# Kernel optimization log

Hardware: AMD Instinct MI355X
Metric: run time of the kernel (lower is better)

The kernel has to match this reference:

```python
import jax, jax.numpy as jnp
import numpy as np

B, S, H, D = 1, 2048, 16, 128
HID = H * D  # 2048
EPS = 1e-6


def setup_inputs() -> dict:
    key = jax.random.key(0)
    ks = jax.random.split(key, 6)
    sc = 1.0 / np.sqrt(HID)
    t = jnp.arange(S, dtype=jnp.float32)[:, None]
    inv = 1.0 / (10000.0 ** (jnp.arange(D // 2, dtype=jnp.float32) / (D // 2)))
    ang = t * inv[None, :]
    return {
        "hidden_states": jax.random.normal(ks[0], (B, S, HID), jnp.float32),
        "freqs_cos": jnp.cos(ang),
        "freqs_sin": jnp.sin(ang),
        "w_qkv": jax.random.normal(ks[1], (HID, 3 * HID), jnp.float32) * sc,
        "b_qkv": jnp.zeros((3 * HID,), jnp.float32),
        "w_norm_q": jnp.ones((HID,), jnp.float32),
        "w_norm_k": jnp.ones((HID,), jnp.float32),
        "w_out": jax.random.normal(ks[2], (HID, HID), jnp.float32) * sc,
        "b_out": jnp.zeros((HID,), jnp.float32),
    }


def _rmsnorm(x, w):
    var = jnp.mean(jnp.square(x), axis=-1, keepdims=True)
    return x * jax.lax.rsqrt(var + EPS) * w


def _rope(x, cos, sin):
    # x: [B, H, S, D]; cos/sin: [S, D//2], interleaved pair rotation
    xr = x.reshape(*x.shape[:-1], D // 2, 2)
    x1, x2 = xr[..., 0], xr[..., 1]
    c = cos[None, None, :, :]
    s = sin[None, None, :, :]
    o1 = x1 * c - x2 * s
    o2 = x1 * s + x2 * c
    return jnp.stack([o1, o2], axis=-1).reshape(x.shape)


def reference(hidden_states, freqs_cos, freqs_sin, w_qkv, b_qkv,
              w_norm_q, w_norm_k, w_out, b_out):
    qkv = hidden_states @ w_qkv + b_qkv  # [B, S, 3*HID]
    q, k, v = jnp.split(qkv, 3, axis=-1)
    q = _rmsnorm(q, w_norm_q).reshape(B, S, H, D).transpose(0, 2, 1, 3)
    k = _rmsnorm(k, w_norm_k).reshape(B, S, H, D).transpose(0, 2, 1, 3)
    v = v.reshape(B, S, H, D).transpose(0, 2, 1, 3)
    q = _rope(q, freqs_cos, freqs_sin)
    k = _rope(k, freqs_cos, freqs_sin)
    scale = 1.0 / np.sqrt(D)
    scores = jnp.einsum("bhqd,bhkd->bhqk", q, k) * scale
    attn = jax.nn.softmax(scores, axis=-1)
    out = jnp.einsum("bhqk,bhkd->bhqd", attn, v)
    out = out.transpose(0, 2, 1, 3).reshape(B, S, HID)
    return out @ w_out + b_out
```

## Files before the change

kernel.cpp:

```cpp
#include <hip/hip_runtime.h>
#include <math.h>

typedef unsigned short u16;
typedef __bf16 bf16x8 __attribute__((ext_vector_type(8)));
typedef float f32x4 __attribute__((ext_vector_type(4)));
typedef unsigned short u16x8 __attribute__((ext_vector_type(8)));

#define SLEN 2048
#define HIDN 2048
#define NH   16
#define DHD  128

static __device__ __forceinline__ float bf2f(u16 u) {
  unsigned int i = ((unsigned int)u) << 16;
  return __builtin_bit_cast(float, i);
}
static __device__ __forceinline__ u16 f2bf(float f) {
  unsigned int x = __builtin_bit_cast(unsigned int, f);
  unsigned int r = x + 0x7fffu + ((x >> 16) & 1u);
  return (u16)(r >> 16);
}
static __device__ __forceinline__ void gload_lds16(const u16* g, u16* l) {
  __builtin_amdgcn_global_load_lds((const __attribute__((address_space(1))) void*)g,
                                   (__attribute__((address_space(3))) void*)l,
                                   16, 0, 0);
}

__global__ __launch_bounds__(256) void prep(const float* __restrict__ wqkv,
                                            const float* __restrict__ wout,
                                            const float* __restrict__ hs,
                                            u16* __restrict__ wqkvT,
                                            u16* __restrict__ woutT,
                                            u16* __restrict__ hsB) {
  const int lin = blockIdx.x;
  const int t = threadIdx.x;
  if (lin >= 4096) {
    int i = ((lin - 4096) * 256 + t) * 8;
    f32x4 a = *(const f32x4*)&hs[i];
    f32x4 b = *(const f32x4*)&hs[i + 4];
    u16x8 v;
#pragma unroll
    for (int j = 0; j < 4; ++j) { v[j] = f2bf(a[j]); v[4 + j] = f2bf(b[j]); }
    *(u16x8*)&hsB[i] = v;
    return;
  }
  const float* in;
  u16* out;
  int istride, ostride, bx, by;
  if (lin < 3072) {
    in = wqkv; out = wqkvT; istride = 6144; ostride = 2048;
    bx = lin & 31; by = lin >> 5;
  } else {
    in = wout; out = woutT; istride = 2048; ostride = 2048;
    int idx = lin - 3072;
    bx = idx & 31; by = idx >> 5;
  }
  __shared__ float tl[64][65];
  const int r0 = bx * 64, c0 = by * 64;
#pragma unroll
  for (int it = 0; it < 4; ++it) {
    int row = it * 16 + (t >> 4);
    int col = (t & 15) * 4;
    f32x4 v = *(const f32x4*)&in[(size_t)(r0 + row) * istride + c0 + col];
    tl[row][col] = v[0]; tl[row][col + 1] = v[1];
    tl[row][col + 2] = v[2]; tl[row][col + 3] = v[3];
  }
  __syncthreads();
#pragma unroll
  for (int it = 0; it < 2; ++it) {
    int orow = it * 32 + (t >> 3);
    int ocol = (t & 7) * 8;
    u16x8 v;
#pragma unroll
    for (int j = 0; j < 8; ++j) v[j] = f2bf(tl[ocol + j][orow]);
    *(u16x8*)&out[(size_t)(c0 + orow) * ostride + r0 + ocol] = v;
  }
}

static __device__ __forceinline__ void xcd_map(int lin, int N, int* pbx, int* pby) {
  const int nby = N >> 7;
  const int cby = nby >> 3;
  const int xcd = lin & 7, idx = lin >> 3;
  *pby = xcd * cby + (idx % cby);
  *pbx = idx / cby;
}

__global__ __launch_bounds__(256) void gemm_sb(const u16* __restrict__ A,
                                               const u16* __restrict__ BT,
                                               const float* __restrict__ bias,
                                               float* Cf, u16* Cb,
                                               int M, int N, int K) {
  int bx, by;
  xcd_map(blockIdx.x, N, &bx, &by);

  __shared__ u16 lA[128 * 64];
  __shared__ u16 lB[128 * 64];
  const int t = threadIdx.x;
  const int lane = t & 63, w = t >> 6;
  const int g = lane >> 4, l16 = lane & 15;
  const int wr = w >> 1, wc = w & 1;
  const u16* Ab = A + (size_t)bx * 128 * K;
  const u16* Bb = BT + (size_t)by * 128 * K;

  f32x4 acc[4][4];
#pragma unroll
  for (int mi = 0; mi < 4; ++mi)
#pragma unroll
    for (int ni = 0; ni < 4; ++ni) acc[mi][ni] = (f32x4)(0.0f);

  for (int k0 = 0; k0 < K; k0 += 64) {
    __syncthreads();
#pragma unroll
    for (int i = 0; i < 4; ++i) {
      int e = t * 8 + i * 2048;
      int row = e >> 6;
      int col16 = (e & 63) >> 3;
      int scol = (col16 ^ (row & 7)) * 8;
      gload_lds16(Ab + (size_t)row * K + k0 + scol, &lA[e]);
      gload_lds16(Bb + (size_t)row * K + k0 + scol, &lB[e]);
    }
    __syncthreads();
#pragma unroll
    for (int kk = 0; kk < 2; ++kk) {
      bf16x8 af[4], bfr[4];
#pragma unroll
      for (int mi = 0; mi < 4; ++mi) {
        int row = wr * 64 + mi * 16 + l16;
        af[mi] = *(const bf16x8*)&lA[row * 64 + (((4 * kk + g) ^ (l16 & 7)) << 3)];
      }
#pragma unroll
      for (int ni = 0; ni < 4; ++ni) {
        int row = wc * 64 + ni * 16 + l16;
        bfr[ni] = *(const bf16x8*)&lB[row * 64 + (((4 * kk + g) ^ (l16 & 7)) << 3)];
      }
#pragma unroll
      for (int mi = 0; mi < 4; ++mi)
#pragma unroll
        for (int ni = 0; ni < 4; ++ni)
          acc[mi][ni] = __builtin_amdgcn_mfma_f32_16x16x32_bf16(af[mi], bfr[ni],
                                                                acc[mi][ni], 0, 0, 0);
    }
  }

#pragma unroll
  for (int ni = 0; ni < 4; ++ni) {
    int n = by * 128 + wc * 64 + ni * 16 + l16;
    float bv = bias[n];
#pragma unroll
    for (int mi = 0; mi < 4; ++mi) {
      int m = bx * 128 + wr * 64 + mi * 16 + 4 * g;
#pragma unroll
      for (int r = 0; r < 4; ++r) {
        float v = acc[mi][ni][r] + bv;
        if (Cf) Cf[(size_t)(m + r) * N + n] = v;
        else    Cb[(size_t)(m + r) * N + n] = f2bf(v);
      }
    }
  }
}

__global__ __launch_bounds__(256) void gemm_db(const u16* __restrict__ A,
                                               const u16* __restrict__ BT,
                                               const float* __restrict__ bias,
                                               float* Cf, u16* Cb,
                                               int M, int N, int K) {
  int bx, by;
  xcd_map(blockIdx.x, N, &bx, &by);

  __shared__ u16 lA[2][128 * 64];
  __shared__ u16 lB[2][128 * 64];
  const int t = threadIdx.x;
  const int lane = t & 63, w = t >> 6;
  const int g = lane >> 4, l16 = lane & 15;
  const int wr = w >> 1, wc = w & 1;
  const u16* Ab = A + (size_t)bx * 128 * K;
  const u16* Bb = BT + (size_t)by * 128 * K;

  f32x4 acc[4][4];
#pragma unroll
  for (int mi = 0; mi < 4; ++mi)
#pragma unroll
    for (int ni = 0; ni < 4; ++ni) acc[mi][ni] = (f32x4)(0.0f);

#pragma unroll
  for (int i = 0; i < 4; ++i) {
    int e = t * 8 + i * 2048;
    int row = e >> 6;
    int col16 = (e & 63) >> 3;
    int scol = (col16 ^ (row & 7)) * 8;
    gload_lds16(Ab + (size_t)row * K + scol, &lA[0][e]);
    gload_lds16(Bb + (size_t)row * K + scol, &lB[0][e]);
  }
  __syncthreads();

  const int nk = K >> 6;
  int cur = 0;
  for (int kt = 0; kt < nk; ++kt) {
    if (kt + 1 < nk) {
      const int k1 = (kt + 1) << 6;
#pragma unroll
      for (int i = 0; i < 4; ++i) {
        int e = t * 8 + i * 2048;
        int row = e >> 6;
        int col16 = (e & 63) >> 3;
        int scol = (col16 ^ (row & 7)) * 8;
        gload_lds16(Ab + (size_t)row * K + k1 + scol, &lA[cur ^ 1][e]);
        gload_lds16(Bb + (size_t)row * K + k1 + scol, &lB[cur ^ 1][e]);
      }
    }
#pragma unroll
    for (int kk = 0; kk < 2; ++kk) {
      bf16x8 af[4], bfr[4];
#pragma unroll
      for (int mi = 0; mi < 4; ++mi) {
        int row = wr * 64 + mi * 16 + l16;
        af[mi] = *(const bf16x8*)&lA[cur][row * 64 + (((4 * kk + g) ^ (l16 & 7)) << 3)];
      }
#pragma unroll
      for (int ni = 0; ni < 4; ++ni) {
        int row = wc * 64 + ni * 16 + l16;
        bfr[ni] = *(const bf16x8*)&lB[cur][row * 64 + (((4 * kk + g) ^ (l16 & 7)) << 3)];
      }
#pragma unroll
      for (int mi = 0; mi < 4; ++mi)
#pragma unroll
        for (int ni = 0; ni < 4; ++ni)
          acc[mi][ni] = __builtin_amdgcn_mfma_f32_16x16x32_bf16(af[mi], bfr[ni],
                                                                acc[mi][ni], 0, 0, 0);
    }
    __syncthreads();
    cur ^= 1;
  }

#pragma unroll
  for (int ni = 0; ni < 4; ++ni) {
    int n = by * 128 + wc * 64 + ni * 16 + l16;
    float bv = bias[n];
#pragma unroll
    for (int mi = 0; mi < 4; ++mi) {
      int m = bx * 128 + wr * 64 + mi * 16 + 4 * g;
#pragma unroll
      for (int r = 0; r < 4; ++r) {
        float v = acc[mi][ni][r] + bv;
        if (Cf) Cf[(size_t)(m + r) * N + n] = v;
        else    Cb[(size_t)(m + r) * N + n] = f2bf(v);
      }
    }
  }
}

__global__ __launch_bounds__(256) void mid(const u16* __restrict__ qkv,
                                           const float* __restrict__ fcos,
                                           const float* __restrict__ fsin,
                                           const float* __restrict__ wq,
                                           const float* __restrict__ wk,
                                           u16* __restrict__ Qr,
                                           u16* __restrict__ Kr,
                                           u16* __restrict__ Vt) {
  const int lin = blockIdx.x;
  const int t = threadIdx.x;

  if (lin >= 2048) {
    __shared__ u16 tl[64][72];
    int idx = lin - 2048;
    int bx = idx & 31;
    int byy = (idx >> 5) & 1;
    int z = idx >> 6;
    const u16* in = qkv + 4096 + (size_t)z * 128;
    u16* out = Vt + (size_t)z * 262144;
    const int r0 = bx * 64, c0 = byy * 64;
#pragma unroll
    for (int it = 0; it < 2; ++it) {
      int row = it * 32 + (t >> 3);
      int col = (t & 7) * 8;
      *(u16x8*)&tl[row][col] =
          *(const u16x8*)&in[(size_t)(r0 + row) * 6144 + c0 + col];
    }
    __syncthreads();
#pragma unroll
    for (int it = 0; it < 2; ++it) {
      int orow = it * 32 + (t >> 3);
      int ocol = (t & 7) * 8;
      u16x8 v;
#pragma unroll
      for (int j = 0; j < 8; ++j) v[j] = tl[ocol + j][orow];
      *(u16x8*)&out[(size_t)(c0 + orow) * 2048 + r0 + ocol] = v;
    }
    return;
  }

  const int s = lin;
  const int lane = t & 63, w = t >> 6;
  __shared__ float red[2][4];
  const u16* row = qkv + (size_t)s * (3 * HIDN);

  u16x8 xq = *(const u16x8*)&row[t * 8];
  u16x8 xk = *(const u16x8*)&row[HIDN + t * 8];
  float fq[8], fk[8];
  float ssq = 0.f, ssk = 0.f;
#pragma unroll
  for (int j = 0; j < 8; ++j) {
    fq[j] = bf2f(xq[j]); ssq += fq[j] * fq[j];
    fk[j] = bf2f(xk[j]); ssk += fk[j] * fk[j];
  }
#pragma unroll
  for (int off = 32; off >= 1; off >>= 1) {
    ssq += __shfl_xor(ssq, off);
    ssk += __shfl_xor(ssk, off);
  }
  if (lane == 0) { red[0][w] = ssq; red[1][w] = ssk; }
  __syncthreads();
  float sq = red[0][0] + red[0][1] + red[0][2] + red[0][3];
  float sk = red[1][0] + red[1][1] + red[1][2] + red[1][3];
  float rq = rsqrtf(sq / (float)HIDN + 1e-6f);
  float rk = rsqrtf(sk / (float)HIDN + 1e-6f);

  f32x4 wq0 = *(const f32x4*)&wq[t * 8];
  f32x4 wq1 = *(const f32x4*)&wq[t * 8 + 4];
  f32x4 wk0 = *(const f32x4*)&wk[t * 8];
  f32x4 wk1 = *(const f32x4*)&wk[t * 8 + 4];
  float wqa[8] = {wq0[0], wq0[1], wq0[2], wq0[3], wq1[0], wq1[1], wq1[2], wq1[3]};
  float wka[8] = {wk0[0], wk0[1], wk0[2], wk0[3], wk1[0], wk1[1], wk1[2], wk1[3]};
  const int c0 = t * 8;
  const int h = c0 >> 7;
  const int d0 = c0 & 127;
  const int i0 = d0 >> 1;
  const float* cp = fcos + (size_t)s * (DHD / 2) + i0;
  const float* sp = fsin + (size_t)s * (DHD / 2) + i0;
  const float qscale = 0.12751744925f;

  u16x8 oq, ok;
#pragma unroll
  for (int p = 0; p < 4; ++p) {
    float c = cp[p], sn = sp[p];
    float q1 = fq[2 * p] * rq * wqa[2 * p];
    float q2 = fq[2 * p + 1] * rq * wqa[2 * p + 1];
    float k1 = fk[2 * p] * rk * wka[2 * p];
    float k2 = fk[2 * p + 1] * rk * wka[2 * p + 1];
    oq[2 * p]     = f2bf((q1 * c - q2 * sn) * qscale);
    oq[2 * p + 1] = f2bf((q1 * sn + q2 * c) * qscale);
    ok[2 * p]     = f2bf(k1 * c - k2 * sn);
    ok[2 * p + 1] = f2bf(k1 * sn + k2 * c);
  }
  size_t o = (size_t)h * SLEN * DHD + (size_t)s * DHD + d0;
  *(u16x8*)&Qr[o] = oq;
  *(u16x8*)&Kr[o] = ok;
}

__global__ __launch_bounds__(256) void attn_fwd(const u16* __restrict__ Qr,
                                                const u16* __restrict__ Kr,
                                                const u16* __restrict__ Vt,
                                                u16* __restrict__ out) {
  const int lin = blockIdx.x;
  const int xcd = lin & 7, idx = lin >> 3;
  const int h = xcd + ((idx >> 5) << 3);
  const int qb = idx & 31;
  const int t = threadIdx.x;
  const int lane = t & 63, w = t >> 6;
  const int g = lane >> 4, l16 = lane & 15;
  const int q0 = qb * 64 + w * 16;
  const u16* Qh = Qr + (size_t)h * SLEN * DHD;
  const u16* Kh = Kr + (size_t)h * SLEN * DHD;
  const u16* Vh = Vt + (size_t)h * DHD * SLEN;

  __shared__ u16 Kl[2][64 * 128];
  __shared__ u16 Vl[2][128 * 64];
  __shared__ u16 Pl[4][16][72];

  bf16x8 aq[4];
#pragma unroll
  for (int dk = 0; dk < 4; ++dk)
    aq[dk] = *(const bf16x8*)&Qh[(size_t)(q0 + l16) * DHD + dk * 32 + g * 8];

  f32x4 o[8];
#pragma unroll
  for (int df = 0; df < 8; ++df) o[df] = (f32x4)(0.0f);
  float m = -INFINITY, lsum = 0.f;

#pragma unroll
  for (int i = 0; i < 4; ++i) {
    int e = t * 8 + i * 2048;
    int kr = e >> 7, kc = (e & 127) >> 3;
    gload_lds16(Kh + (size_t)kr * DHD + ((kc ^ (kr & 7)) << 3), &Kl[0][e]);
    int vr = e >> 6, vc = (e & 63) >> 3;
    gload_lds16(Vh + (size_t)vr * SLEN + ((vc ^ (vr & 7)) << 3), &Vl[0][e]);
  }
  __syncthreads();

  int cur = 0;
  for (int kt = 0; kt < SLEN / 64; ++kt) {
    if (kt + 1 < SLEN / 64) {
      const int kv1 = (kt + 1) * 64;
#pragma unroll
      for (int i = 0; i < 4; ++i) {
        int e = t * 8 + i * 2048;
        int kr = e >> 7, kc = (e & 127) >> 3;
        gload_lds16(Kh + (size_t)(kv1 + kr) * DHD + ((kc ^ (kr & 7)) << 3),
                    &Kl[cur ^ 1][e]);
        int vr = e >> 6, vc = (e & 63) >> 3;
        gload_lds16(Vh + (size_t)vr * SLEN + kv1 + ((vc ^ (vr & 7)) << 3),
                    &Vl[cur ^ 1][e]);
      }
    }

    f32x4 s4[4];
#pragma unroll
    for (int nf = 0; nf < 4; ++nf) s4[nf] = (f32x4)(0.0f);
    __builtin_amdgcn_s_setprio(1);
#pragma unroll
    for (int nf = 0; nf < 4; ++nf) {
#pragma unroll
      for (int dk = 0; dk < 4; ++dk) {
        bf16x8 bk = *(const bf16x8*)&Kl[cur][(nf * 16 + l16) * 128 +
                                            (((dk * 4 + g) ^ (l16 & 7)) << 3)];
        s4[nf] = __builtin_amdgcn_mfma_f32_16x16x32_bf16(bk, aq[dk], s4[nf], 0, 0, 0);
      }
    }
    __builtin_amdgcn_s_setprio(0);
    float tm = s4[0][0];
#pragma unroll
    for (int nf = 0; nf < 4; ++nf)
#pragma unroll
      for (int r = 0; r < 4; ++r) tm = fmaxf(tm, s4[nf][r]);
    tm = fmaxf(tm, __shfl_xor(tm, 16));
    tm = fmaxf(tm, __shfl_xor(tm, 32));
    const bool nogrow = (tm <= m);
    const float mn = nogrow ? m : tm;
    float ls = 0.f;
#pragma unroll
    for (int nf = 0; nf < 4; ++nf)
#pragma unroll
      for (int r = 0; r < 4; ++r) {
        float p = exp2f(s4[nf][r] - mn);
        s4[nf][r] = p;
        ls += p;
      }
    ls += __shfl_xor(ls, 16);
    ls += __shfl_xor(ls, 32);
    if (__all(nogrow)) {
      lsum += ls;
    } else {
      float corr = exp2f(m - mn);
      m = mn;
      lsum = lsum * corr + ls;
#pragma unroll
      for (int r = 0; r < 4; ++r) {
        float cr = __shfl(corr, 20 * g + r);
#pragma unroll
        for (int df = 0; df < 8; ++df) o[df][r] *= cr;
      }
    }
#pragma unroll
    for (int nf = 0; nf < 4; ++nf)
#pragma unroll
      for (int r = 0; r < 4; ++r)
        Pl[w][l16][nf * 16 + 4 * g + r] = f2bf(s4[nf][r]);
#pragma unroll
    for (int ks = 0; ks < 2; ++ks) {
      bf16x8 ap = *(const bf16x8*)&Pl[w][l16][ks * 32 + g * 8];
      __builtin_amdgcn_s_setprio(1);
#pragma unroll
      for (int df = 0; df < 8; ++df) {
        bf16x8 bv = *(const bf16x8*)&Vl[cur][(df * 16 + l16) * 64 +
                                             (((ks * 4 + g) ^ (l16 & 7)) << 3)];
        o[df] = __builtin_amdgcn_mfma_f32_16x16x32_bf16(ap, bv, o[df], 0, 0, 0);
      }
      __builtin_amdgcn_s_setprio(0);
    }
    __syncthreads();
    cur ^= 1;
  }

  const float invq = 1.0f / lsum;
#pragma unroll
  for (int r = 0; r < 4; ++r) {
    float ir = __shfl(invq, 20 * g + r);
#pragma unroll
    for (int df = 0; df < 8; ++df)
      out[(size_t)(q0 + 4 * g + r) * HIDN + h * DHD + df * 16 + l16] =
          f2bf(o[df][r] * ir);
  }
}

extern "C" void kernel_launch(void* const* d_in, const int* in_sizes, int n_in,
                              void* d_out, int out_size, void* d_ws, size_t ws_size,
                              hipStream_t stream) {
  (void)in_sizes; (void)n_in; (void)out_size; (void)ws_size;
  const float* hs   = (const float*)d_in[0];
  const float* fc   = (const float*)d_in[1];
  const float* fs   = (const float*)d_in[2];
  const float* wqkv = (const float*)d_in[3];
  const float* bqkv = (const float*)d_in[4];
  const float* wnq  = (const float*)d_in[5];
  const float* wnk  = (const float*)d_in[6];
  const float* wout = (const float*)d_in[7];
  const float* bout = (const float*)d_in[8];
  float* out = (float*)d_out;
  char* ws = (char*)d_ws;

  u16* wqkvT = (u16*)(ws);
  u16* woutT = (u16*)(ws + 25165824);
  u16* qkv   = (u16*)(ws + 33554432);
  u16* hsB   = (u16*)(ws + 58720256);
  u16* Qr    = (u16*)(ws + 58720256);
  u16* Kr    = (u16*)(ws + 67108864);
  u16* Vt    = (u16*)(ws + 75497472);
  u16* attnO = (u16*)(ws + 83886080);

  prep<<<dim3(6144), 256, 0, stream>>>(wqkv, wout, hs, wqkvT, woutT, hsB);
  gemm_sb<<<dim3(768), 256, 0, stream>>>(hsB, wqkvT, bqkv, nullptr, qkv,
                                         2048, 6144, 2048);
  mid<<<dim3(3072), 256, 0, stream>>>(qkv, fc, fs, wnq, wnk, Qr, Kr, Vt);
  attn_fwd<<<dim3(512), 256, 0, stream>>>(Qr, Kr, Vt, attnO);
  gemm_db<<<dim3(256), 256, 0, stream>>>(attnO, woutT, bout, out, nullptr,
                                         2048, 2048, 2048);
}
```

Baseline: 201.4 us.

## Split attention over two KV halves and merge partials in a combine kernel

The attention kernel now splits each query block's key/value range into two halves, launching twice as many blocks, and writes unnormalized partial outputs plus per-row max and sum. A new combine kernel merges the two partials with a log-sum-exp style rescale. The double-buffered LDS prefetch is replaced by single-buffered loads with two barriers per tile, which cuts LDS use (more resident blocks) but removes load/compute overlap. It also adds an extra launch and extra global traffic for the partials, and stores the partials in bf16 before the merge.

```diff
diff --git a/kernel.cpp b/kernel.cpp
--- a/kernel.cpp
+++ b/kernel.cpp
@@ -347,24 +347,27 @@
   *(u16x8*)&Kr[o] = ok;
 }
 
-__global__ __launch_bounds__(256) void attn_fwd(const u16* __restrict__ Qr,
-                                                const u16* __restrict__ Kr,
-                                                const u16* __restrict__ Vt,
-                                                u16* __restrict__ out) {
+__global__ __launch_bounds__(256) void attn_split(const u16* __restrict__ Qr,
+                                                  const u16* __restrict__ Kr,
+                                                  const u16* __restrict__ Vt,
+                                                  u16* __restrict__ Op,
+                                                  float* __restrict__ ml) {
   const int lin = blockIdx.x;
   const int xcd = lin & 7, idx = lin >> 3;
-  const int h = xcd + ((idx >> 5) << 3);
-  const int qb = idx & 31;
+  const int split = idx & 1;
+  const int qb = (idx >> 1) & 31;
+  const int h = xcd + ((idx >> 6) << 3);
   const int t = threadIdx.x;
   const int lane = t & 63, w = t >> 6;
   const int g = lane >> 4, l16 = lane & 15;
   const int q0 = qb * 64 + w * 16;
+  const int kvbase = split << 10;
   const u16* Qh = Qr + (size_t)h * SLEN * DHD;
   const u16* Kh = Kr + (size_t)h * SLEN * DHD;
   const u16* Vh = Vt + (size_t)h * DHD * SLEN;
 
-  __shared__ u16 Kl[2][64 * 128];
-  __shared__ u16 Vl[2][128 * 64];
+  __shared__ u16 Kl[64 * 128];
+  __shared__ u16 Vl[128 * 64];
   __shared__ u16 Pl[4][16][72];
 
   bf16x8 aq[4];
@@ -377,31 +380,18 @@
   for (int df = 0; df < 8; ++df) o[df] = (f32x4)(0.0f);
   float m = -INFINITY, lsum = 0.f;
 
-#pragma unroll
-  for (int i = 0; i < 4; ++i) {
-    int e = t * 8 + i * 2048;
-    int kr = e >> 7, kc = (e & 127) >> 3;
-    gload_lds16(Kh + (size_t)kr * DHD + ((kc ^ (kr & 7)) << 3), &Kl[0][e]);
-    int vr = e >> 6, vc = (e & 63) >> 3;
-    gload_lds16(Vh + (size_t)vr * SLEN + ((vc ^ (vr & 7)) << 3), &Vl[0][e]);
-  }
-  __syncthreads();
-
-  int cur = 0;
-  for (int kt = 0; kt < SLEN / 64; ++kt) {
-    if (kt + 1 < SLEN / 64) {
-      const int kv1 = (kt + 1) * 64;
-#pragma unroll
-      for (int i = 0; i < 4; ++i) {
-        int e = t * 8 + i * 2048;
-        int kr = e >> 7, kc = (e & 127) >> 3;
-        gload_lds16(Kh + (size_t)(kv1 + kr) * DHD + ((kc ^ (kr & 7)) << 3),
-                    &Kl[cur ^ 1][e]);
-        int vr = e >> 6, vc = (e & 63) >> 3;
-        gload_lds16(Vh + (size_t)vr * SLEN + kv1 + ((vc ^ (vr & 7)) << 3),
-                    &Vl[cur ^ 1][e]);
-      }
-    }
+  for (int kt = 0; kt < 16; ++kt) {
+    const int kv0 = kvbase + kt * 64;
+    __syncthreads();
+#pragma unroll
+    for (int i = 0; i < 4; ++i) {
+      int e = t * 8 + i * 2048;
+      int kr = e >> 7, kc = (e & 127) >> 3;
+      gload_lds16(Kh + (size_t)(kv0 + kr) * DHD + ((kc ^ (kr & 7)) << 3), &Kl[e]);
+      int vr = e >> 6, vc = (e & 63) >> 3;
+      gload_lds16(Vh + (size_t)vr * SLEN + kv0 + ((vc ^ (vr & 7)) << 3), &Vl[e]);
+    }
+    __syncthreads();
 
     f32x4 s4[4];
 #pragma unroll
@@ -411,8 +401,8 @@
     for (int nf = 0; nf < 4; ++nf) {
 #pragma unroll
       for (int dk = 0; dk < 4; ++dk) {
-        bf16x8 bk = *(const bf16x8*)&Kl[cur][(nf * 16 + l16) * 128 +
-                                            (((dk * 4 + g) ^ (l16 & 7)) << 3)];
+        bf16x8 bk = *(const bf16x8*)&Kl[(nf * 16 + l16) * 128 +
+                                        (((dk * 4 + g) ^ (l16 & 7)) << 3)];
         s4[nf] = __builtin_amdgcn_mfma_f32_16x16x32_bf16(bk, aq[dk], s4[nf], 0, 0, 0);
       }
     }
@@ -461,25 +451,46 @@
       __builtin_amdgcn_s_setprio(1);
 #pragma unroll
       for (int df = 0; df < 8; ++df) {
-        bf16x8 bv = *(const bf16x8*)&Vl[cur][(df * 16 + l16) * 64 +
-                                             (((ks * 4 + g) ^ (l16 & 7)) << 3)];
+        bf16x8 bv = *(const bf16x8*)&Vl[(df * 16 + l16) * 64 +
+                                        (((ks * 4 + g) ^ (l16 & 7)) << 3)];
         o[df] = __builtin_amdgcn_mfma_f32_16x16x32_bf16(ap, bv, o[df], 0, 0, 0);
       }
       __builtin_amdgcn_s_setprio(0);
     }
-    __syncthreads();
-    cur ^= 1;
-  }
-
-  const float invq = 1.0f / lsum;
-#pragma unroll
-  for (int r = 0; r < 4; ++r) {
-    float ir = __shfl(invq, 20 * g + r);
+  }
+
+  const size_t ob = ((size_t)split * NH + h) * SLEN * DHD;
+#pragma unroll
+  for (int r = 0; r < 4; ++r)
 #pragma unroll
     for (int df = 0; df < 8; ++df)
-      out[(size_t)(q0 + 4 * g + r) * HIDN + h * DHD + df * 16 + l16] =
-          f2bf(o[df][r] * ir);
-  }
+      Op[ob + (size_t)(q0 + 4 * g + r) * DHD + df * 16 + l16] = f2bf(o[df][r]);
+  if (g == 0) {
+    size_t mb = (((size_t)split * NH + h) * SLEN + (q0 + l16)) * 2;
+    ml[mb] = m;
+    ml[mb + 1] = lsum;
+  }
+}
+
+__global__ __launch_bounds__(256) void combine(const u16* __restrict__ Op,
+                                               const float* __restrict__ ml,
+                                               u16* __restrict__ attnO) {
+  const int q = blockIdx.x, t = threadIdx.x;
+  const int h = t >> 4, d0 = (t & 15) * 8;
+  size_t mb0 = (((size_t)0 * NH + h) * SLEN + q) * 2;
+  size_t mb1 = (((size_t)1 * NH + h) * SLEN + q) * 2;
+  float m0 = ml[mb0], l0 = ml[mb0 + 1];
+  float m1 = ml[mb1], l1 = ml[mb1 + 1];
+  float ms = fmaxf(m0, m1);
+  float w0 = exp2f(m0 - ms), w1 = exp2f(m1 - ms);
+  float inv = 1.0f / (l0 * w0 + l1 * w1);
+  u16x8 a = *(const u16x8*)&Op[((size_t)0 * NH + h) * SLEN * DHD + (size_t)q * DHD + d0];
+  u16x8 b = *(const u16x8*)&Op[((size_t)1 * NH + h) * SLEN * DHD + (size_t)q * DHD + d0];
+  u16x8 v;
+#pragma unroll
+  for (int j = 0; j < 8; ++j)
+    v[j] = f2bf((bf2f(a[j]) * w0 + bf2f(b[j]) * w1) * inv);
+  *(u16x8*)&attnO[(size_t)q * HIDN + h * DHD + d0] = v;
 }
 
 extern "C" void kernel_launch(void* const* d_in, const int* in_sizes, int n_in,
@@ -506,12 +517,15 @@
   u16* Kr    = (u16*)(ws + 67108864);
   u16* Vt    = (u16*)(ws + 75497472);
   u16* attnO = (u16*)(ws + 83886080);
+  float* mlF = (float*)(ws);
+  u16* Op    = (u16*)(ws + 33554432);
 
   prep<<<dim3(6144), 256, 0, stream>>>(wqkv, wout, hs, wqkvT, woutT, hsB);
   gemm_sb<<<dim3(768), 256, 0, stream>>>(hsB, wqkvT, bqkv, nullptr, qkv,
                                          2048, 6144, 2048);
   mid<<<dim3(3072), 256, 0, stream>>>(qkv, fc, fs, wnq, wnk, Qr, Kr, Vt);
-  attn_fwd<<<dim3(512), 256, 0, stream>>>(Qr, Kr, Vt, attnO);
+  attn_split<<<dim3(1024), 256, 0, stream>>>(Qr, Kr, Vt, Op, mlF);
+  combine<<<dim3(2048), 256, 0, stream>>>(Op, mlF, attnO);
   gemm_db<<<dim3(256), 256, 0, stream>>>(attnO, woutT, bout, out, nullptr,
                                          2048, 2048, 2048);
 }
```

Measured after the change: 215.0 us. 6.8% more time.

## Double-buffer QKV GEMM LDS tiles with BK=32 prefetch pipeline

Applied to the files above, without the earlier changes.

Replaces the single-buffered BK=64 QKV projection GEMM with a double-buffered BK=32 version. The global-to-LDS loads for the next k-tile are issued before the MFMAs on the current tile, and the loop needs one barrier per iteration instead of two. The aim is to hide global load latency behind compute. In exchange there are twice as many k iterations, each doing half the MFMA work per barrier, and the swizzle becomes a 4-way XOR that may cause more LDS bank conflicts.

```diff
diff --git a/kernel.cpp b/kernel.cpp
--- a/kernel.cpp
+++ b/kernel.cpp
@@ -85,16 +85,16 @@
   *pbx = idx / cby;
 }
 
-__global__ __launch_bounds__(256) void gemm_sb(const u16* __restrict__ A,
-                                               const u16* __restrict__ BT,
-                                               const float* __restrict__ bias,
-                                               float* Cf, u16* Cb,
-                                               int M, int N, int K) {
+__global__ __launch_bounds__(256) void gemm_p32(const u16* __restrict__ A,
+                                                const u16* __restrict__ BT,
+                                                const float* __restrict__ bias,
+                                                float* Cf, u16* Cb,
+                                                int M, int N, int K) {
   int bx, by;
   xcd_map(blockIdx.x, N, &bx, &by);
 
-  __shared__ u16 lA[128 * 64];
-  __shared__ u16 lB[128 * 64];
+  __shared__ u16 lA[2][128 * 32];
+  __shared__ u16 lB[2][128 * 32];
   const int t = threadIdx.x;
   const int lane = t & 63, w = t >> 6;
   const int g = lane >> 4, l16 = lane & 15;
@@ -108,38 +108,51 @@
 #pragma unroll
     for (int ni = 0; ni < 4; ++ni) acc[mi][ni] = (f32x4)(0.0f);
 
-  for (int k0 = 0; k0 < K; k0 += 64) {
+#pragma unroll
+  for (int i = 0; i < 2; ++i) {
+    int e = t * 8 + i * 2048;
+    int row = e >> 5;
+    int c4 = (e & 31) >> 3;
+    int scol = (c4 ^ (row & 3)) * 8;
+    gload_lds16(Ab + (size_t)row * K + scol, &lA[0][e]);
+    gload_lds16(Bb + (size_t)row * K + scol, &lB[0][e]);
+  }
+  __syncthreads();
+
+  const int nk = K >> 5;
+  int cur = 0;
+  for (int kt = 0; kt < nk; ++kt) {
+    if (kt + 1 < nk) {
+      const int k1 = (kt + 1) << 5;
+#pragma unroll
+      for (int i = 0; i < 2; ++i) {
+        int e = t * 8 + i * 2048;
+        int row = e >> 5;
+        int c4 = (e & 31) >> 3;
+        int scol = (c4 ^ (row & 3)) * 8;
+        gload_lds16(Ab + (size_t)row * K + k1 + scol, &lA[cur ^ 1][e]);
+        gload_lds16(Bb + (size_t)row * K + k1 + scol, &lB[cur ^ 1][e]);
+      }
+    }
+    bf16x8 af[4], bfr[4];
+#pragma unroll
+    for (int mi = 0; mi < 4; ++mi) {
+      int row = wr * 64 + mi * 16 + l16;
+      af[mi] = *(const bf16x8*)&lA[cur][row * 32 + ((g ^ (row & 3)) << 3)];
+    }
+#pragma unroll
+    for (int ni = 0; ni < 4; ++ni) {
+      int row = wc * 64 + ni * 16 + l16;
+      bfr[ni] = *(const bf16x8*)&lB[cur][row * 32 + ((g ^ (row & 3)) << 3)];
+    }
+#pragma unroll
+    for (int mi = 0; mi < 4; ++mi)
+#pragma unroll
+      for (int ni = 0; ni < 4; ++ni)
+        acc[mi][ni] = __builtin_amdgcn_mfma_f32_16x16x32_bf16(af[mi], bfr[ni],
+                                                              acc[mi][ni], 0, 0, 0);
     __syncthreads();
-#pragma unroll
-    for (int i = 0; i < 4; ++i) {
-      int e = t * 8 + i * 2048;
-      int row = e >> 6;
-      int col16 = (e & 63) >> 3;
-      int scol = (col16 ^ (row & 7)) * 8;
-      gload_lds16(Ab + (size_t)row * K + k0 + scol, &lA[e]);
-      gload_lds16(Bb + (size_t)row * K + k0 + scol, &lB[e]);
-    }
-    __syncthreads();
-#pragma unroll
-    for (int kk = 0; kk < 2; ++kk) {
-      bf16x8 af[4], bfr[4];
-#pragma unroll
-      for (int mi = 0; mi < 4; ++mi) {
-        int row = wr * 64 + mi * 16 + l16;
-        af[mi] = *(const bf16x8*)&lA[row * 64 + (((4 * kk + g) ^ (l16 & 7)) << 3)];
-      }
-#pragma unroll
-      for (int ni = 0; ni < 4; ++ni) {
-        int row = wc * 64 + ni * 16 + l16;
-        bfr[ni] = *(const bf16x8*)&lB[row * 64 + (((4 * kk + g) ^ (l16 & 7)) << 3)];
-      }
-#pragma unroll
-      for (int mi = 0; mi < 4; ++mi)
-#pragma unroll
-        for (int ni = 0; ni < 4; ++ni)
-          acc[mi][ni] = __builtin_amdgcn_mfma_f32_16x16x32_bf16(af[mi], bfr[ni],
-                                                                acc[mi][ni], 0, 0, 0);
-    }
+    cur ^= 1;
   }
 
 #pragma unroll
@@ -508,8 +521,8 @@
   u16* attnO = (u16*)(ws + 83886080);
 
   prep<<<dim3(6144), 256, 0, stream>>>(wqkv, wout, hs, wqkvT, woutT, hsB);
-  gemm_sb<<<dim3(768), 256, 0, stream>>>(hsB, wqkvT, bqkv, nullptr, qkv,
-                                         2048, 6144, 2048);
+  gemm_p32<<<dim3(768), 256, 0, stream>>>(hsB, wqkvT, bqkv, nullptr, qkv,
+                                          2048, 6144, 2048);
   mid<<<dim3(3072), 256, 0, stream>>>(qkv, fc, fs, wnq, wnk, Qr, Kr, Vt);
   attn_fwd<<<dim3(512), 256, 0, stream>>>(Qr, Kr, Vt, attnO);
   gemm_db<<<dim3(256), 256, 0, stream>>>(attnO, woutT, bout, out, nullptr,
```

After: 202.7 us. Within noise of the previous version (+0.6%).
